# Kernel tuning notes

Measured on AMD Instinct MI355X. Metric: run time of the kernel, lower is better.

## Reference

```python
import jax, jax.numpy as jnp
import numpy as np

B, N, D, H = 2, 2048, 1024, 16
DK = D // H


def setup_inputs() -> dict:
    key = jax.random.key(0)
    ks = jax.random.split(key, 12)
    s = D ** -0.5
    inp = {
        "query": jax.random.normal(ks[0], (B, N, D), jnp.float32),
        "key": jax.random.normal(ks[1], (B, N, D), jnp.float32),
        "value": jax.random.normal(ks[2], (B, N, D), jnp.float32),
        # causal mask: 1 = keep, 0 = masked (matches create_causal_mask)
        "mask": jnp.tril(jnp.ones((N, N), jnp.int32)),
        "Wq": jax.random.normal(ks[3], (D, D), jnp.float32) * s,
        "bq": jnp.zeros((D,), jnp.float32),
        "Wk": jax.random.normal(ks[4], (D, D), jnp.float32) * s,
        "bk": jnp.zeros((D,), jnp.float32),
        "Wv": jax.random.normal(ks[5], (D, D), jnp.float32) * s,
        "bv": jnp.zeros((D,), jnp.float32),
        "Wo": jax.random.normal(ks[6], (D, D), jnp.float32) * s,
        "bo": jnp.zeros((D,), jnp.float32),
    }
    return inp


def reference(query, key, value, mask, Wq, bq, Wk, bk, Wv, bv, Wo, bo):
    scale = DK ** -0.5
    # Linear projections (torch nn.Linear: x @ W.T + b), split into heads -> [B,H,N,DK]
    q = (query @ Wq.T + bq).reshape(B, N, H, DK).transpose(0, 2, 1, 3)
    k = (key @ Wk.T + bk).reshape(B, N, H, DK).transpose(0, 2, 1, 3)
    v = (value @ Wv.T + bv).reshape(B, N, H, DK).transpose(0, 2, 1, 3)
    scores = jnp.einsum("bhqd,bhkd->bhqk", q, k) * scale  # [B,H,N,N]
    scores = jnp.where(mask[None, None, :, :] == 0, jnp.float32(-1e9), scores)
    attn = jax.nn.softmax(scores, axis=-1)
    ctx = jnp.einsum("bhqk,bhkd->bhqd", attn, v)  # [B,H,N,DK]
    ctx = ctx.transpose(0, 2, 1, 3).reshape(B, N, D)
    return ctx @ Wo.T + bo
```

## Files before the change

### kernel.cpp

```cpp
#include <hip/hip_runtime.h>
#include <hip/hip_bf16.h>

typedef __attribute__((ext_vector_type(4))) float f32x4;
typedef __attribute__((ext_vector_type(8))) __bf16 bf16x8;
typedef __attribute__((ext_vector_type(8))) unsigned short u16x8;
typedef __attribute__((ext_vector_type(4))) unsigned short u16x4;
typedef unsigned short u16;

#define DEV static __device__ __forceinline__

DEV u16 f2bf(float f){
  unsigned u = __builtin_bit_cast(unsigned, f);
  u += 0x7fff + ((u >> 16) & 1);
  return (u16)(u >> 16);
}

DEV f32x4 mfma16(bf16x8 a, bf16x8 b, f32x4 c){
  return __builtin_amdgcn_mfma_f32_16x16x32_bf16(a, b, c, 0, 0, 0);
}

DEV void gload16(const void* g, void* l){
  __builtin_amdgcn_global_load_lds((const __attribute__((address_space(1))) void*)g,
                                   (__attribute__((address_space(3))) void*)l,
                                   16, 0, 0);
}

DEV float fexp2(float x){
#if __has_builtin(__builtin_amdgcn_exp2f)
  return __builtin_amdgcn_exp2f(x);
#else
  float r; asm("v_exp_f32 %0, %1" : "=v"(r) : "v"(x)); return r;
#endif
}

__global__ __launch_bounds__(256) void cvt_k(
    const float* __restrict__ s0, const float* __restrict__ s1,
    const float* __restrict__ s2, const float* __restrict__ s3,
    const float* __restrict__ s4, const float* __restrict__ s5,
    const float* __restrict__ s6,
    u16* __restrict__ d0, u16* __restrict__ d1, u16* __restrict__ d2,
    u16* __restrict__ d3, u16* __restrict__ d4, u16* __restrict__ d5,
    u16* __restrict__ d6){
  const int y = blockIdx.y;
  const float* __restrict__ s = y==0?s0:y==1?s1:y==2?s2:y==3?s3:y==4?s4:y==5?s5:s6;
  u16* __restrict__ d         = y==0?d0:y==1?d1:y==2?d2:y==3?d3:y==4?d4:y==5?d5:d6;
  const int n8 = (y < 3) ? (4096*1024/8) : (1024*1024/8);
  for (int i = blockIdx.x*256 + threadIdx.x; i < n8; i += gridDim.x*256){
    f32x4 a = *(const f32x4*)&s[(size_t)i*8];
    f32x4 b = *(const f32x4*)&s[(size_t)i*8 + 4];
    u16x8 h;
    #pragma unroll
    for (int j = 0; j < 4; ++j){ h[j] = f2bf(a[j]); h[j+4] = f2bf(b[j]); }
    *(u16x8*)&d[(size_t)i*8] = h;
  }
}

template<int OUT_F32>
__global__ __launch_bounds__(256) void gemm_bt(
    const u16* __restrict__ A0, const u16* __restrict__ A1, const u16* __restrict__ A2,
    const u16* __restrict__ B0, const u16* __restrict__ B1, const u16* __restrict__ B2,
    const float* __restrict__ e0, const float* __restrict__ e1, const float* __restrict__ e2,
    void* __restrict__ C0, void* __restrict__ C1, void* __restrict__ C2){
  __shared__ u16 As[128*32];
  __shared__ u16 Bs[128*32];
  const int z = blockIdx.z;
  const u16* __restrict__ A    = z==0 ? A0 : z==1 ? A1 : A2;
  const u16* __restrict__ Bw   = z==0 ? B0 : z==1 ? B1 : B2;
  const float* __restrict__ bias = z==0 ? e0 : z==1 ? e1 : e2;
  void* __restrict__ Cp        = z==0 ? C0 : z==1 ? C1 : C2;
  const bool vt = (OUT_F32 == 0) && (z == 2);

  const int tid  = threadIdx.x;
  const int lane = tid & 63, w = tid >> 6;
  const int wr = w >> 1, wc = w & 1;
  const int l16 = lane & 15, lhi = lane >> 4;
  const int bm = vt ? blockIdx.x : blockIdx.y;
  const int bn = vt ? blockIdx.y : blockIdx.x;

  const int srow = w*16 + (lane >> 2);
  const int scol = (lane & 3)*8;
  const u16* Asrc = A  + (size_t)(bm*128 + srow)*1024 + scol;
  const u16* Bsrc = Bw + (size_t)(bn*128 + srow)*1024 + scol;
  u16* Adst0 = As + w*512;
  u16* Bdst0 = Bs + w*512;

  f32x4 acc[4][4] = {};

  for (int k0 = 0; k0 < 1024; k0 += 32){
    __syncthreads();
    gload16(Asrc + k0,             Adst0);
    gload16(Asrc + 64*1024 + k0,   Adst0 + 2048);
    gload16(Bsrc + k0,             Bdst0);
    gload16(Bsrc + 64*1024 + k0,   Bdst0 + 2048);
    __syncthreads();

    bf16x8 af[4], bfr[4];
    #pragma unroll
    for (int mi = 0; mi < 4; ++mi)
      af[mi] = *(const bf16x8*)&As[(wr*64 + mi*16 + l16)*32 + lhi*8];
    #pragma unroll
    for (int nf = 0; nf < 4; ++nf)
      bfr[nf] = *(const bf16x8*)&Bs[(wc*64 + nf*16 + l16)*32 + lhi*8];
    #pragma unroll
    for (int mi = 0; mi < 4; ++mi)
      #pragma unroll
      for (int nf = 0; nf < 4; ++nf)
        acc[mi][nf] = mfma16(af[mi], bfr[nf], acc[mi][nf]);
  }

  #pragma unroll
  for (int mi = 0; mi < 4; ++mi){
    #pragma unroll
    for (int nf = 0; nf < 4; ++nf){
      int row0 = bm*128 + wr*64 + mi*16 + lhi*4;
      int col  = bn*128 + wc*64 + nf*16 + l16;
      float bc = bias[col];
      #pragma unroll
      for (int r = 0; r < 4; ++r){
        int row = row0 + r;
        float val = acc[mi][nf][r] + (vt ? bias[row] : bc);
        if (OUT_F32){
          ((float*)Cp)[(size_t)row*1024 + col] = val;
        } else if (!vt){
          int b = row >> 11, n = row & 2047;
          int h = col >> 6,  dk = col & 63;
          ((u16*)Cp)[(((size_t)(b*16 + h))*2048 + n)*64 + dk] = f2bf(val);
        } else {
          int h = row >> 6,  dk = row & 63;
          int b = col >> 11, n = col & 2047;
          ((u16*)Cp)[(((size_t)(b*16 + h))*64 + dk)*2048 + n] = f2bf(val);
        }
      }
    }
  }
}

#define SCL 0.18033688011f
#define THR 11.0f
#define PLD 72

DEV void proc_tile(int t, int qt, int q_abs,
                   const u16* __restrict__ Ksb, const u16* __restrict__ Vsb,
                   u16* __restrict__ PsW,
                   bf16x8 bq0, bf16x8 bq1,
                   f32x4* ctx, float& m_r, float& l_r,
                   int l16, int lhi, int lane, int swz){
  f32x4 s4[4] = {};
  #pragma unroll
  for (int nf = 0; nf < 4; ++nf){
    bf16x8 ak0 = *(const bf16x8*)&Ksb[(nf*16 + l16)*64 + ((lhi*8) ^ swz)];
    bf16x8 ak1 = *(const bf16x8*)&Ksb[(nf*16 + l16)*64 + ((32 + lhi*8) ^ swz)];
    s4[nf] = mfma16(ak0, bq0, s4[nf]);
    s4[nf] = mfma16(ak1, bq1, s4[nf]);
  }

  const bool domask = (t == qt);
  float mt = -3.0e38f;
  #pragma unroll
  for (int nf = 0; nf < 4; ++nf)
    #pragma unroll
    for (int r = 0; r < 4; ++r){
      float x = s4[nf][r] * SCL;
      if (domask){
        int kc = t*64 + nf*16 + lhi*4 + r;
        x = (kc > q_abs) ? -1.0e30f : x;
      }
      s4[nf][r] = x;
      mt = fmaxf(mt, x);
    }
  mt = fmaxf(mt, __shfl_xor(mt, 16));
  mt = fmaxf(mt, __shfl_xor(mt, 32));

  if (!__all(mt <= m_r + THR)){
    float mn = fmaxf(m_r, mt);
    float sf = fexp2(m_r - mn);
    m_r = mn;
    l_r *= sf;
    float sfb[4];
    #pragma unroll
    for (int r = 0; r < 4; ++r)
      sfb[r] = __shfl(sf, (lane >> 4)*4 + r);
    #pragma unroll
    for (int dkf = 0; dkf < 4; ++dkf)
      #pragma unroll
      for (int r = 0; r < 4; ++r)
        ctx[dkf][r] *= sfb[r];
  }

  float lt = 0.f;
  #pragma unroll
  for (int nf = 0; nf < 4; ++nf){
    u16x4 hq;
    #pragma unroll
    for (int r = 0; r < 4; ++r){
      float p = fexp2(s4[nf][r] - m_r);
      unsigned u = __builtin_bit_cast(unsigned, p) & 0xffff0000u;
      lt += __builtin_bit_cast(float, u);
      hq[r] = (u16)(u >> 16);
    }
    *(u16x4*)&PsW[l16*PLD + nf*16 + lhi*4] = hq;
  }
  lt += __shfl_xor(lt, 16);
  lt += __shfl_xor(lt, 32);
  l_r += lt;

  #pragma unroll
  for (int ks = 0; ks < 2; ++ks){
    bf16x8 pa = *(const bf16x8*)&PsW[l16*PLD + ks*32 + lhi*8];
    #pragma unroll
    for (int dkf = 0; dkf < 4; ++dkf){
      bf16x8 vb = *(const bf16x8*)&Vsb[(dkf*16 + l16)*64 + ((ks*32 + lhi*8) ^ swz)];
      ctx[dkf] = mfma16(pa, vb, ctx[dkf]);
    }
  }
}

__global__ __launch_bounds__(256) void attn_k(const u16* __restrict__ Q,
                                              const u16* __restrict__ K,
                                              const u16* __restrict__ Vt,
                                              u16* __restrict__ CTX){
  __shared__ u16 Ks[2][64*64];
  __shared__ u16 Vs[2][64*64];
  __shared__ u16 Ps[4][2][16*PLD];
  const int tid  = threadIdx.x;
  const int lane = tid & 63, w = tid >> 6;
  const int l16 = lane & 15, lhi = lane >> 4;
  const int f  = blockIdx.x;
  const int bh = f & 31, xp = f >> 5;
  const size_t base = (size_t)bh * 2048 * 64;
  const u16* Qb = Q  + base;
  const u16* Kb = K  + base;
  const u16* Vb = Vt + base;
  const int b = bh >> 4, h = bh & 15;

  const int s0 = tid, s1 = tid + 256;
  const int r0 = s0 >> 3, c0 = ((s0 & 7) ^ (r0 & 7))*8;
  const int r1 = s1 >> 3, c1 = ((s1 & 7) ^ (r1 & 7))*8;
  const u16* Ksrc0 = Kb + r0*64 + c0;
  const u16* Ksrc1 = Kb + r1*64 + c1;
  const u16* Vsrc0 = Vb + (size_t)r0*2048 + c0;
  const u16* Vsrc1 = Vb + (size_t)r1*2048 + c1;
  const int swz = (l16 & 7)*8;

  const int qtA = xp,      ntA = xp + 1;
  const int qtB = 31 - xp, ntB = 32 - xp;
  const int qaA = qtA*64 + w*16 + l16;
  const int qaB = qtB*64 + w*16 + l16;

  bf16x8 bqA0 = *(const bf16x8*)&Qb[(size_t)qaA*64 + lhi*8];
  bf16x8 bqA1 = *(const bf16x8*)&Qb[(size_t)qaA*64 + 32 + lhi*8];
  bf16x8 bqB0 = *(const bf16x8*)&Qb[(size_t)qaB*64 + lhi*8];
  bf16x8 bqB1 = *(const bf16x8*)&Qb[(size_t)qaB*64 + 32 + lhi*8];

  f32x4 ctxA[4] = {}, ctxB[4] = {};
  float mA = -3.0e38f, lA = 0.f, mB = -3.0e38f, lB = 0.f;

  u16* PsA = &Ps[w][0][0];
  u16* PsB = &Ps[w][1][0];

  gload16(Ksrc0, &Ks[0][s0*8]);  gload16(Ksrc1, &Ks[0][s1*8]);
  gload16(Vsrc0, &Vs[0][s0*8]);  gload16(Vsrc1, &Vs[0][s1*8]);
  __syncthreads();

  int cur = 0;
  int t = 0;
  for (; t < ntA; ++t){
    if (t + 1 < ntB){
      int nb = cur ^ 1;
      gload16(Ksrc0 + (t+1)*4096, &Ks[nb][s0*8]);
      gload16(Ksrc1 + (t+1)*4096, &Ks[nb][s1*8]);
      gload16(Vsrc0 + (t+1)*64,   &Vs[nb][s0*8]);
      gload16(Vsrc1 + (t+1)*64,   &Vs[nb][s1*8]);
    }
    proc_tile(t, qtB, qaB, Ks[cur], Vs[cur], PsB, bqB0, bqB1,
              ctxB, mB, lB, l16, lhi, lane, swz);
    proc_tile(t, qtA, qaA, Ks[cur], Vs[cur], PsA, bqA0, bqA1,
              ctxA, mA, lA, l16, lhi, lane, swz);
    __syncthreads();
    cur ^= 1;
  }
  for (; t < ntB; ++t){
    if (t + 1 < ntB){
      int nb = cur ^ 1;
      gload16(Ksrc0 + (t+1)*4096, &Ks[nb][s0*8]);
      gload16(Ksrc1 + (t+1)*4096, &Ks[nb][s1*8]);
      gload16(Vsrc0 + (t+1)*64,   &Vs[nb][s0*8]);
      gload16(Vsrc1 + (t+1)*64,   &Vs[nb][s1*8]);
    }
    proc_tile(t, qtB, qaB, Ks[cur], Vs[cur], PsB, bqB0, bqB1,
              ctxB, mB, lB, l16, lhi, lane, swz);
    __syncthreads();
    cur ^= 1;
  }

  float lfA[4], lfB[4];
  #pragma unroll
  for (int r = 0; r < 4; ++r){
    lfA[r] = __shfl(lA, (lane >> 4)*4 + r);
    lfB[r] = __shfl(lB, (lane >> 4)*4 + r);
  }
  #pragma unroll
  for (int dkf = 0; dkf < 4; ++dkf)
    #pragma unroll
    for (int r = 0; r < 4; ++r){
      int qA = qtA*64 + w*16 + lhi*4 + r;
      int qB = qtB*64 + w*16 + lhi*4 + r;
      CTX[((size_t)(b*2048 + qA))*1024 + h*64 + dkf*16 + l16] = f2bf(ctxA[dkf][r] / lfA[r]);
      CTX[((size_t)(b*2048 + qB))*1024 + h*64 + dkf*16 + l16] = f2bf(ctxB[dkf][r] / lfB[r]);
    }
}

constexpr int LDP = 40;

__global__ __launch_bounds__(256) void gemm_qkv(
    const float* __restrict__ Aq, const float* __restrict__ Ak, const float* __restrict__ Av,
    const float* __restrict__ Bq, const float* __restrict__ Bk, const float* __restrict__ Bv,
    const float* __restrict__ eq, const float* __restrict__ ek, const float* __restrict__ ev,
    u16* __restrict__ Oq, u16* __restrict__ Ok, u16* __restrict__ Ov){
  __shared__ u16 As[128][LDP];
  __shared__ u16 Bs[128][LDP];
  const int z = blockIdx.z;
  const float* __restrict__ A   = z == 0 ? Aq : z == 1 ? Ak : Av;
  const float* __restrict__ W   = z == 0 ? Bq : z == 1 ? Bk : Bv;
  const float* __restrict__ bias= z == 0 ? eq : z == 1 ? ek : ev;
  u16* __restrict__ C           = z == 0 ? Oq : z == 1 ? Ok : Ov;
  const bool vt = (z == 2);

  const int tid  = threadIdx.x;
  const int lane = tid & 63, wv = tid >> 6;
  const int wr = wv >> 1, wc = wv & 1;
  const int l16 = lane & 15, lhi = lane >> 4;
  const int bm = vt ? blockIdx.x : blockIdx.y;
  const int bn = vt ? blockIdx.y : blockIdx.x;
  const int K = 1024;

  f32x4 acc[4][4] = {};

  for (int k0 = 0; k0 < K; k0 += 32){
    __syncthreads();
    #pragma unroll
    for (int j = 0; j < 4; ++j){
      int s = tid + j*256;
      int row = s >> 3, c4 = s & 7;
      f32x4 v = *(const f32x4*)&A[(size_t)(bm*128 + row)*K + k0 + c4*4];
      u16x4 hh;
      #pragma unroll
      for (int i = 0; i < 4; ++i) hh[i] = f2bf(v[i]);
      *(u16x4*)&As[row][c4*4] = hh;
    }
    #pragma unroll
    for (int j = 0; j < 4; ++j){
      int s = tid + j*256;
      int row = s >> 3, c4 = s & 7;
      f32x4 v = *(const f32x4*)&W[(size_t)(bn*128 + row)*K + k0 + c4*4];
      u16x4 hh;
      #pragma unroll
      for (int i = 0; i < 4; ++i) hh[i] = f2bf(v[i]);
      *(u16x4*)&Bs[row][c4*4] = hh;
    }
    __syncthreads();

    bf16x8 af[4], bfr[4];
    #pragma unroll
    for (int mi = 0; mi < 4; ++mi)
      af[mi] = *(const bf16x8*)&As[wr*64 + mi*16 + l16][lhi*8];
    #pragma unroll
    for (int nf = 0; nf < 4; ++nf)
      bfr[nf] = *(const bf16x8*)&Bs[wc*64 + nf*16 + l16][lhi*8];
    #pragma unroll
    for (int mi = 0; mi < 4; ++mi)
      #pragma unroll
      for (int nf = 0; nf < 4; ++nf)
        acc[mi][nf] = mfma16(af[mi], bfr[nf], acc[mi][nf]);
  }

  #pragma unroll
  for (int mi = 0; mi < 4; ++mi){
    #pragma unroll
    for (int nf = 0; nf < 4; ++nf){
      int row0 = bm*128 + wr*64 + mi*16 + lhi*4;
      int col  = bn*128 + wc*64 + nf*16 + l16;
      float bc = bias[col];
      #pragma unroll
      for (int r = 0; r < 4; ++r){
        int row = row0 + r;
        float val = acc[mi][nf][r] + (vt ? bias[row] : bc);
        if (!vt){
          int b = row >> 11, n = row & 2047;
          int h = col >> 6,  dk = col & 63;
          C[(((size_t)(b*16 + h))*2048 + n)*64 + dk] = f2bf(val);
        } else {
          int h = row >> 6,  dk = row & 63;
          int b = col >> 11, n = col & 2047;
          C[(((size_t)(b*16 + h))*64 + dk)*2048 + n] = f2bf(val);
        }
      }
    }
  }
}

__global__ __launch_bounds__(256) void gemm_o_fb(const u16* __restrict__ A,
                                                 const float* __restrict__ W,
                                                 const float* __restrict__ bias,
                                                 float* __restrict__ C){
  __shared__ u16 As[128][LDP];
  __shared__ u16 Bs[64][LDP];
  const int tid  = threadIdx.x;
  const int lane = tid & 63, wv = tid >> 6;
  const int wr = wv >> 1, wc = wv & 1;
  const int l16 = lane & 15, lhi = lane >> 4;
  const int bm = blockIdx.y, bn = blockIdx.x;
  const int K = 1024;

  f32x4 acc[4][2] = {};

  for (int k0 = 0; k0 < K; k0 += 32){
    __syncthreads();
    #pragma unroll
    for (int j = 0; j < 2; ++j){
      int s = tid + j*256;
      int row = s >> 2, c8 = s & 3;
      *(u16x8*)&As[row][c8*8] =
          *(const u16x8*)&A[(size_t)(bm*128 + row)*K + k0 + c8*8];
    }
    #pragma unroll
    for (int j = 0; j < 2; ++j){
      int s = tid + j*256;
      int row = s >> 3, c4 = s & 7;
      f32x4 v = *(const f32x4*)&W[(size_t)(bn*64 + row)*K + k0 + c4*4];
      u16x4 hh;
      #pragma unroll
      for (int i = 0; i < 4; ++i) hh[i] = f2bf(v[i]);
      *(u16x4*)&Bs[row][c4*4] = hh;
    }
    __syncthreads();

    bf16x8 af[4], bfr[2];
    #pragma unroll
    for (int mi = 0; mi < 4; ++mi)
      af[mi] = *(const bf16x8*)&As[wr*64 + mi*16 + l16][lhi*8];
    #pragma unroll
    for (int nf = 0; nf < 2; ++nf)
      bfr[nf] = *(const bf16x8*)&Bs[wc*32 + nf*16 + l16][lhi*8];
    #pragma unroll
    for (int mi = 0; mi < 4; ++mi)
      #pragma unroll
      for (int nf = 0; nf < 2; ++nf)
        acc[mi][nf] = mfma16(af[mi], bfr[nf], acc[mi][nf]);
  }

  #pragma unroll
  for (int mi = 0; mi < 4; ++mi){
    #pragma unroll
    for (int nf = 0; nf < 2; ++nf){
      int row0 = bm*128 + wr*64 + mi*16 + lhi*4;
      int col  = bn*64 + wc*32 + nf*16 + l16;
      float bv = bias[col];
      #pragma unroll
      for (int r = 0; r < 4; ++r)
        C[(size_t)(row0 + r)*1024 + col] = acc[mi][nf][r] + bv;
    }
  }
}

extern "C" void kernel_launch(void* const* d_in, const int* in_sizes, int n_in,
                              void* d_out, int out_size, void* d_ws, size_t ws_size,
                              hipStream_t stream){
  const float* q  = (const float*)d_in[0];
  const float* k  = (const float*)d_in[1];
  const float* v  = (const float*)d_in[2];
  const float* Wq = (const float*)d_in[4];  const float* bq = (const float*)d_in[5];
  const float* Wk = (const float*)d_in[6];  const float* bk = (const float*)d_in[7];
  const float* Wv = (const float*)d_in[8];  const float* bv = (const float*)d_in[9];
  const float* Wo = (const float*)d_in[10]; const float* bo = (const float*)d_in[11];
  float* out = (float*)d_out;
  dim3 blk(256);

  const size_t need = (size_t)(3*4194304 + 4*1048576 + 3*4194304) * 2;
  if (ws_size >= need){
    u16* Xqb = (u16*)d_ws;
    u16* Xkb = Xqb + 4194304;
    u16* Xvb = Xkb + 4194304;
    u16* Wqb = Xvb + 4194304;
    u16* Wkb = Wqb + 1048576;
    u16* Wvb = Wkb + 1048576;
    u16* Wob = Wvb + 1048576;
    u16* Qw  = Wob + 1048576;
    u16* Kw  = Qw + 4194304;
    u16* Vw  = Kw + 4194304;
    u16* Cw  = Xqb;

    cvt_k<<<dim3(512, 7), blk, 0, stream>>>(q, k, v, Wq, Wk, Wv, Wo,
                                            Xqb, Xkb, Xvb, Wqb, Wkb, Wvb, Wob);
    gemm_bt<0><<<dim3(8, 32, 3), blk, 0, stream>>>(
        Xqb, Xkb, Wvb, Wqb, Wkb, Xvb, bq, bk, bv,
        (void*)Qw, (void*)Kw, (void*)Vw);
    attn_k<<<dim3(512), blk, 0, stream>>>(Qw, Kw, Vw, Cw);
    gemm_bt<1><<<dim3(8, 32, 1), blk, 0, stream>>>(
        Cw, Cw, Cw, Wob, Wob, Wob, bo, bo, bo,
        (void*)out, (void*)out, (void*)out);
  } else {
    u16* Qw = (u16*)d_ws;
    u16* Kw = Qw + (size_t)4096*1024;
    u16* Vw = Kw + (size_t)4096*1024;
    u16* Cw = Vw + (size_t)4096*1024;
    gemm_qkv<<<dim3(8, 32, 3), blk, 0, stream>>>(q, k, Wv, Wq, Wk, v, bq, bk, bv,
                                                 Qw, Kw, Vw);
    attn_k<<<dim3(512), blk, 0, stream>>>(Qw, Kw, Vw, Cw);
    gemm_o_fb<<<dim3(16, 32), blk, 0, stream>>>(Cw, Wo, bo, out);
  }
}
```

Before: 137.3 us.

## Fold softmax scale into Q projection and split attention tile into softmax/PV phases

Multiplies the Q projection output by the softmax scale (times log2 e) inside the QKV GEMM epilogues, so the attention inner loop no longer scales every score. The per-tile work is split into a softmax phase and a PV phase, and the two query tiles are interleaved so both QK/softmax stages run before both PV MFMA stages. The PV phase raises wave priority with s_setprio. Probability packing uses v_perm to truncate to bf16, and the row-max is computed as a tree reduction. Scaling Q before the bf16 rounding changes numerics slightly, and the interleaving keeps more live registers.

```diff
diff --git a/kernel.cpp b/kernel.cpp
--- a/kernel.cpp
+++ b/kernel.cpp
@@ -5,6 +5,7 @@
 typedef __attribute__((ext_vector_type(8))) __bf16 bf16x8;
 typedef __attribute__((ext_vector_type(8))) unsigned short u16x8;
 typedef __attribute__((ext_vector_type(4))) unsigned short u16x4;
+typedef __attribute__((ext_vector_type(2))) unsigned int u32x2;
 typedef unsigned short u16;
 
 #define DEV static __device__ __forceinline__
@@ -55,6 +56,10 @@
   }
 }
 
+#define SCL 0.18033688011f
+#define THR 11.0f
+#define PLD 72
+
 template<int OUT_F32>
 __global__ __launch_bounds__(256) void gemm_bt(
     const u16* __restrict__ A0, const u16* __restrict__ A1, const u16* __restrict__ A2,
@@ -69,6 +74,7 @@
   const float* __restrict__ bias = z==0 ? e0 : z==1 ? e1 : e2;
   void* __restrict__ Cp        = z==0 ? C0 : z==1 ? C1 : C2;
   const bool vt = (OUT_F32 == 0) && (z == 2);
+  const float qs = (OUT_F32 == 0 && z == 0) ? SCL : 1.0f;
 
   const int tid  = threadIdx.x;
   const int lane = tid & 63, w = tid >> 6;
@@ -118,7 +124,7 @@
       #pragma unroll
       for (int r = 0; r < 4; ++r){
         int row = row0 + r;
-        float val = acc[mi][nf][r] + (vt ? bias[row] : bc);
+        float val = (acc[mi][nf][r] + (vt ? bias[row] : bc)) * qs;
         if (OUT_F32){
           ((float*)Cp)[(size_t)row*1024 + col] = val;
         } else if (!vt){
@@ -135,16 +141,11 @@
   }
 }
 
-#define SCL 0.18033688011f
-#define THR 11.0f
-#define PLD 72
-
-DEV void proc_tile(int t, int qt, int q_abs,
-                   const u16* __restrict__ Ksb, const u16* __restrict__ Vsb,
-                   u16* __restrict__ PsW,
-                   bf16x8 bq0, bf16x8 bq1,
-                   f32x4* ctx, float& m_r, float& l_r,
-                   int l16, int lhi, int lane, int swz){
+DEV void sm_tile(int t, int qt, int q_abs,
+                 const u16* __restrict__ Ksb, u16* __restrict__ PsW,
+                 bf16x8 bq0, bf16x8 bq1,
+                 f32x4* ctx, float& m_r, float& l_r,
+                 int l16, int lhi, int lane, int swz){
   f32x4 s4[4] = {};
   #pragma unroll
   for (int nf = 0; nf < 4; ++nf){
@@ -154,20 +155,21 @@
     s4[nf] = mfma16(ak1, bq1, s4[nf]);
   }
 
-  const bool domask = (t == qt);
-  float mt = -3.0e38f;
-  #pragma unroll
-  for (int nf = 0; nf < 4; ++nf)
-    #pragma unroll
-    for (int r = 0; r < 4; ++r){
-      float x = s4[nf][r] * SCL;
-      if (domask){
+  if (t == qt){
+    #pragma unroll
+    for (int nf = 0; nf < 4; ++nf)
+      #pragma unroll
+      for (int r = 0; r < 4; ++r){
         int kc = t*64 + nf*16 + lhi*4 + r;
-        x = (kc > q_abs) ? -1.0e30f : x;
+        if (kc > q_abs) s4[nf][r] = -1.0e30f;
       }
-      s4[nf][r] = x;
-      mt = fmaxf(mt, x);
-    }
+  }
+
+  float mt = fmaxf(
+      fmaxf(fmaxf(fmaxf(s4[0][0],s4[0][1]), fmaxf(s4[0][2],s4[0][3])),
+            fmaxf(fmaxf(s4[1][0],s4[1][1]), fmaxf(s4[1][2],s4[1][3]))),
+      fmaxf(fmaxf(fmaxf(s4[2][0],s4[2][1]), fmaxf(s4[2][2],s4[2][3])),
+            fmaxf(fmaxf(s4[3][0],s4[3][1]), fmaxf(s4[3][2],s4[3][3]))));
   mt = fmaxf(mt, __shfl_xor(mt, 16));
   mt = fmaxf(mt, __shfl_xor(mt, 32));
 
@@ -188,31 +190,40 @@
   }
 
   float lt = 0.f;
+  u16* prow = PsW + l16*PLD;
   #pragma unroll
   for (int nf = 0; nf < 4; ++nf){
-    u16x4 hq;
-    #pragma unroll
-    for (int r = 0; r < 4; ++r){
-      float p = fexp2(s4[nf][r] - m_r);
-      unsigned u = __builtin_bit_cast(unsigned, p) & 0xffff0000u;
-      lt += __builtin_bit_cast(float, u);
-      hq[r] = (u16)(u >> 16);
-    }
-    *(u16x4*)&PsW[l16*PLD + nf*16 + lhi*4] = hq;
+    float p0 = fexp2(s4[nf][0] - m_r);
+    float p1 = fexp2(s4[nf][1] - m_r);
+    float p2 = fexp2(s4[nf][2] - m_r);
+    float p3 = fexp2(s4[nf][3] - m_r);
+    lt += (p0 + p1) + (p2 + p3);
+    unsigned w0 = __builtin_amdgcn_perm(__builtin_bit_cast(unsigned, p1),
+                                        __builtin_bit_cast(unsigned, p0), 0x07060302u);
+    unsigned w1 = __builtin_amdgcn_perm(__builtin_bit_cast(unsigned, p3),
+                                        __builtin_bit_cast(unsigned, p2), 0x07060302u);
+    u32x2 wp = {w0, w1};
+    *(u32x2*)&prow[nf*16 + lhi*4] = wp;
   }
   lt += __shfl_xor(lt, 16);
   lt += __shfl_xor(lt, 32);
   l_r += lt;
-
+}
+
+DEV void pv_tile(const u16* __restrict__ Vsb, const u16* __restrict__ PsW,
+                 f32x4* ctx, int l16, int lhi, int swz){
+  const u16* prow = PsW + l16*PLD;
+  __builtin_amdgcn_s_setprio(1);
   #pragma unroll
   for (int ks = 0; ks < 2; ++ks){
-    bf16x8 pa = *(const bf16x8*)&PsW[l16*PLD + ks*32 + lhi*8];
+    bf16x8 pa = *(const bf16x8*)&prow[ks*32 + lhi*8];
     #pragma unroll
     for (int dkf = 0; dkf < 4; ++dkf){
       bf16x8 vb = *(const bf16x8*)&Vsb[(dkf*16 + l16)*64 + ((ks*32 + lhi*8) ^ swz)];
       ctx[dkf] = mfma16(pa, vb, ctx[dkf]);
     }
   }
+  __builtin_amdgcn_s_setprio(0);
 }
 
 __global__ __launch_bounds__(256) void attn_k(const u16* __restrict__ Q,
@@ -272,10 +283,10 @@
       gload16(Vsrc0 + (t+1)*64,   &Vs[nb][s0*8]);
       gload16(Vsrc1 + (t+1)*64,   &Vs[nb][s1*8]);
     }
-    proc_tile(t, qtB, qaB, Ks[cur], Vs[cur], PsB, bqB0, bqB1,
-              ctxB, mB, lB, l16, lhi, lane, swz);
-    proc_tile(t, qtA, qaA, Ks[cur], Vs[cur], PsA, bqA0, bqA1,
-              ctxA, mA, lA, l16, lhi, lane, swz);
+    sm_tile(t, qtB, qaB, Ks[cur], PsB, bqB0, bqB1, ctxB, mB, lB, l16, lhi, lane, swz);
+    sm_tile(t, qtA, qaA, Ks[cur], PsA, bqA0, bqA1, ctxA, mA, lA, l16, lhi, lane, swz);
+    pv_tile(Vs[cur], PsB, ctxB, l16, lhi, swz);
+    pv_tile(Vs[cur], PsA, ctxA, l16, lhi, swz);
     __syncthreads();
     cur ^= 1;
   }
@@ -287,8 +298,8 @@
       gload16(Vsrc0 + (t+1)*64,   &Vs[nb][s0*8]);
       gload16(Vsrc1 + (t+1)*64,   &Vs[nb][s1*8]);
     }
-    proc_tile(t, qtB, qaB, Ks[cur], Vs[cur], PsB, bqB0, bqB1,
-              ctxB, mB, lB, l16, lhi, lane, swz);
+    sm_tile(t, qtB, qaB, Ks[cur], PsB, bqB0, bqB1, ctxB, mB, lB, l16, lhi, lane, swz);
+    pv_tile(Vs[cur], PsB, ctxB, l16, lhi, swz);
     __syncthreads();
     cur ^= 1;
   }
@@ -325,6 +336,7 @@
   const float* __restrict__ bias= z == 0 ? eq : z == 1 ? ek : ev;
   u16* __restrict__ C           = z == 0 ? Oq : z == 1 ? Ok : Ov;
   const bool vt = (z == 2);
+  const float qs = (z == 0) ? SCL : 1.0f;
 
   const int tid  = threadIdx.x;
   const int lane = tid & 63, wv = tid >> 6;
@@ -384,7 +396,7 @@
       #pragma unroll
       for (int r = 0; r < 4; ++r){
         int row = row0 + r;
-        float val = acc[mi][nf][r] + (vt ? bias[row] : bc);
+        float val = (acc[mi][nf][r] + (vt ? bias[row] : bc)) * qs;
         if (!vt){
           int b = row >> 11, n = row & 2047;
           int h = col >> 6,  dk = col & 63;
```

Result: faster. 132.5 us (-3.5%).
